# Kernel tuning notes

Hardware: AMD Instinct MI355X
Metric: run time of the kernel (lower is better)

Reference implementation:

```python
import jax, jax.numpy as jnp
import numpy as np

L = 2048      # max_length / encoder sequence length
E = 1024      # eo_hidden_size
H = 1024      # hidden_size
D = 512       # embed_size
V = 32000     # vocab_size
MV = 32768    # max_vocab_size


def setup_inputs() -> dict:
    key = jax.random.key(0)
    ks = jax.random.split(key, 20)
    s = 0.02
    return {
        "inp": jax.random.randint(ks[0], (1,), 0, V),
        "hidden": jax.random.normal(ks[1], (1, 1, H), jnp.float32),
        "encoder_outputs": jax.random.normal(ks[2], (L, E), jnp.float32),
        "input_seq": jax.random.randint(ks[3], (L,), 0, MV),
        "pre_prob": jax.random.randint(ks[4], (L,), 0, 2),
        "emb": jax.random.normal(ks[5], (V, D), jnp.float32) * s,
        "attn_W": jax.random.normal(ks[6], (L, H + D), jnp.float32) * s,
        "attn_b": jnp.zeros((L,), jnp.float32),
        "comb_W": jax.random.normal(ks[7], (H, E + D), jnp.float32) * s,
        "comb_b": jnp.zeros((H,), jnp.float32),
        "W_ih": jax.random.normal(ks[8], (3 * H, H + E), jnp.float32) * s,
        "W_hh": jax.random.normal(ks[9], (3 * H, H), jnp.float32) * s,
        "b_ih": jnp.zeros((3 * H,), jnp.float32),
        "b_hh": jnp.zeros((3 * H,), jnp.float32),
        "Wo_W": jax.random.normal(ks[10], (V, H), jnp.float32) * s,
        "Wo_b": jnp.zeros((V,), jnp.float32),
        "Wc_W": jax.random.normal(ks[11], (H, E), jnp.float32) * s,
        "Wc_b": jnp.zeros((H,), jnp.float32),
    }


def reference(inp, hidden, encoder_outputs, input_seq, pre_prob,
              emb, attn_W, attn_b, comb_W, comb_b,
              W_ih, W_hh, b_ih, b_hh, Wo_W, Wo_b, Wc_W, Wc_b):
    tok = inp[0]
    # --- copy-mechanism selective read (int path, matches torch .long() trunc) ---
    sel_w = (input_seq == tok).astype(jnp.int32) * pre_prob.astype(jnp.int32)  # [L]
    eo_int = jax.lax.stop_gradient(encoder_outputs).astype(jnp.int32)          # trunc toward 0
    sel_reading = (sel_w @ eo_int).astype(jnp.float32)                          # [E]
    # --- embedding (OOV -> UNK id 2); dropout is identity in eval ---
    embed_idx = jnp.where(tok >= V, 2, tok)
    embedded = emb[embed_idx]                                                   # [D]
    h = hidden[0, 0]                                                            # [H]
    # --- attention over encoder outputs ---
    attn_weights = jax.nn.softmax(attn_W @ jnp.concatenate([embedded, h]) + attn_b)  # [L]
    attn_applied = attn_weights @ encoder_outputs                               # [E]
    out = jax.nn.relu(comb_W @ jnp.concatenate([embedded, attn_applied]) + comb_b)   # [H]
    # --- single GRU step (torch gate order: r, z, n) ---
    x = jnp.concatenate([out, sel_reading])                                     # [H+E]
    gi = W_ih @ x + b_ih
    gh = W_hh @ h + b_hh
    r = jax.nn.sigmoid(gi[:H] + gh[:H])
    z = jax.nn.sigmoid(gi[H:2 * H] + gh[H:2 * H])
    n = jnp.tanh(gi[2 * H:] + r * gh[2 * H:])
    h_new = (1.0 - z) * n + z * h                                               # [H]
    # --- generate vs copy scores ---
    score_g = Wo_W @ h_new + Wo_b                                               # [V]
    score_c = jnp.tanh(encoder_outputs @ Wc_W.T + Wc_b) @ h_new                 # [L]
    score = jax.nn.softmax(jnp.concatenate([score_g, score_c]))                 # [V+L]
    prob_g, prob_c = score[:V], score[V:]
    # pad generate probs to MV and scatter-add copy probs (== mm with one-hot)
    out1 = jnp.zeros((MV,), score.dtype).at[:V].set(prob_g)
    out1 = out1.at[input_seq].add(prob_c)
    out1 = jnp.where(out1 == 0, 1e-9, out1)
    out1 = out1.at[2].set(1e-9)
    out1 = jnp.log(out1)
    return (out1[None, :], h_new[None, None, :], attn_weights[None, :], prob_c[None, :])
```

## Files before the change

### kernel.cpp

```cpp
#include <hip/hip_runtime.h>
#include <math.h>

#define LQ 2048
#define EQ 1024
#define HQ 1024
#define DQ 512
#define VQ 32000
#define MVQ 32768

#define OUT1_OFF 0
#define HNEW_OFF 32768
#define AW_OFF   33792
#define PC_OFF   35840

#define PSZ 2097152

typedef __attribute__((ext_vector_type(8))) short short8_t;
typedef __attribute__((ext_vector_type(8))) unsigned short ushort8_t;
typedef __attribute__((ext_vector_type(4))) float floatx4;

__device__ inline float wred(float v) {
    v += __shfl_down(v, 32);
    v += __shfl_down(v, 16);
    v += __shfl_down(v, 8);
    v += __shfl_down(v, 4);
    v += __shfl_down(v, 2);
    v += __shfl_down(v, 1);
    return v;
}
__device__ inline float wred_max(float v) {
    v = fmaxf(v, __shfl_down(v, 32));
    v = fmaxf(v, __shfl_down(v, 16));
    v = fmaxf(v, __shfl_down(v, 8));
    v = fmaxf(v, __shfl_down(v, 4));
    v = fmaxf(v, __shfl_down(v, 2));
    v = fmaxf(v, __shfl_down(v, 1));
    return v;
}
__device__ inline float sigmoidf_(float x) { return 1.0f / (1.0f + expf(-x)); }
__device__ inline unsigned short f2bf(float x) {
    unsigned int u = __float_as_uint(x);
    unsigned int r = (u + 0x7fffu + ((u >> 16) & 1u)) >> 16;
    return (unsigned short)r;
}
__device__ inline float bf2f(unsigned short b) {
    return __uint_as_float(((unsigned int)b) << 16);
}
__device__ __forceinline__ void gload16(const unsigned short* g,
                                        unsigned short* l) {
    __builtin_amdgcn_global_load_lds(
        (const __attribute__((address_space(1))) unsigned int*)g,
        (__attribute__((address_space(3))) unsigned int*)l, 16, 0, 0);
}

__global__ __launch_bounds__(256) void k_split_prep(
    const float* __restrict__ enc, const float* __restrict__ Wc,
    const int* __restrict__ inp, const int* __restrict__ input_seq,
    const int* __restrict__ pre_prob,
    unsigned short* __restrict__ Ah, unsigned short* __restrict__ Al,
    unsigned short* __restrict__ Bh, unsigned short* __restrict__ Bl,
    float* __restrict__ x2)
{
    __shared__ int s_cnt;
    __shared__ int s_list[LQ];
    int tid = threadIdx.x;
    if (blockIdx.x == 1536) {
        if (tid == 0) s_cnt = 0;
        __syncthreads();
        int tok = inp[0];
        for (int l = tid; l < LQ; l += 256) {
            if (input_seq[l] == tok && pre_prob[l] != 0) {
                int p = atomicAdd(&s_cnt, 1);
                s_list[p] = l;
            }
        }
        __syncthreads();
        int nm = s_cnt;
        for (int e = tid; e < EQ; e += 256) {
            int acc = 0;
            for (int j = 0; j < nm; ++j)
                acc += (int)enc[(size_t)s_list[j] * EQ + e];
            x2[HQ + e] = (float)acc;
        }
        return;
    }
    size_t e0 = ((size_t)blockIdx.x * 256 + tid) * 8;
    const float* src;
    unsigned short *hdst, *ldst;
    size_t off;
    if (e0 < (size_t)LQ * EQ) { src = enc; hdst = Ah; ldst = Al; off = e0; }
    else { src = Wc; hdst = Bh; ldst = Bl; off = e0 - (size_t)LQ * EQ; }
    float4 v0 = *(const float4*)(src + off);
    float4 v1 = *(const float4*)(src + off + 4);
    float vv[8] = {v0.x, v0.y, v0.z, v0.w, v1.x, v1.y, v1.z, v1.w};
    ushort8_t H, L;
    #pragma unroll
    for (int k = 0; k < 8; ++k) {
        float x = vv[k];
        unsigned short hb = f2bf(x);
        H[k] = hb;
        L[k] = f2bf(x - bf2f(hb));
    }
    *(ushort8_t*)(hdst + off) = H;
    *(ushort8_t*)(ldst + off) = L;
}

__global__ __launch_bounds__(256, 2) void k_gemm_mfma(
    const unsigned short* __restrict__ Ah, const unsigned short* __restrict__ Al,
    const unsigned short* __restrict__ Bh, const unsigned short* __restrict__ Bl,
    float* __restrict__ P)
{
    __shared__ unsigned short sm[4 * 8192];
    const int t = threadIdx.x;
    const int lane = t & 63, wid = t >> 6;
    const int n0 = blockIdx.x * 128;
    const int m0 = blockIdx.y * 128;
    const int kz = blockIdx.z * 512;
    float* Pz = P + (size_t)blockIdx.z * PSZ;

    const unsigned short* tsrc =
        (wid == 0) ? Ah + (size_t)m0 * EQ :
        (wid == 1) ? Al + (size_t)m0 * EQ :
        (wid == 2) ? Bh + (size_t)n0 * EQ :
                     Bl + (size_t)n0 * EQ;
    unsigned short* tdst = sm + wid * 8192;

    const int srow = lane >> 3;
    const int schunk = lane & 7;
    const int wm = (wid >> 1) * 64, wn = (wid & 1) * 64;
    const int fr = lane & 15, kg = lane >> 4;

    floatx4 acc[4][4];
    #pragma unroll
    for (int i = 0; i < 4; ++i)
        #pragma unroll
        for (int j = 0; j < 4; ++j)
            acc[i][j] = (floatx4){0.f, 0.f, 0.f, 0.f};

    for (int s = 0; s < 8; ++s) {
        #pragma unroll
        for (int c = 0; c < 16; ++c) {
            int row = c * 8 + srow;
            int gch = schunk ^ (row & 7);
            gload16(tsrc + (size_t)row * EQ + kz + s * 64 + gch * 8,
                    tdst + c * 512);
        }
        __syncthreads();
        #pragma unroll
        for (int kk = 0; kk < 2; ++kk) {
            short8_t fah[4], fal[4], fbh[4], fbl[4];
            #pragma unroll
            for (int f = 0; f < 4; ++f) {
                int rowa = wm + f * 16 + fr;
                int ba = rowa * 128 + ((kk * 4 + kg) ^ (rowa & 7)) * 16;
                fah[f] = *(const short8_t*)((const char*)sm + ba);
                fal[f] = *(const short8_t*)((const char*)sm + 16384 + ba);
                int rowb = wn + f * 16 + fr;
                int bb = rowb * 128 + ((kk * 4 + kg) ^ (rowb & 7)) * 16;
                fbh[f] = *(const short8_t*)((const char*)sm + 32768 + bb);
                fbl[f] = *(const short8_t*)((const char*)sm + 49152 + bb);
            }
            #pragma unroll
            for (int i = 0; i < 4; ++i)
                #pragma unroll
                for (int j = 0; j < 4; ++j) {
                    acc[i][j] = __builtin_amdgcn_mfma_f32_16x16x32_bf16(
                        fah[i], fbh[j], acc[i][j], 0, 0, 0);
                    acc[i][j] = __builtin_amdgcn_mfma_f32_16x16x32_bf16(
                        fal[i], fbh[j], acc[i][j], 0, 0, 0);
                    acc[i][j] = __builtin_amdgcn_mfma_f32_16x16x32_bf16(
                        fah[i], fbl[j], acc[i][j], 0, 0, 0);
                }
        }
        __syncthreads();
    }
    #pragma unroll
    for (int i = 0; i < 4; ++i)
        #pragma unroll
        for (int j = 0; j < 4; ++j) {
            int row = m0 + wm + i * 16 + kg * 4;
            int col = n0 + wn + j * 16 + fr;
            #pragma unroll
            for (int r = 0; r < 4; ++r)
                Pz[(size_t)(row + r) * HQ + col] = acc[i][j][r];
        }
}

__global__ __launch_bounds__(256) void k_attn(
    const float* __restrict__ W, const float* __restrict__ b,
    const int* __restrict__ inp, const float* __restrict__ emb,
    const float* __restrict__ hidden, float* __restrict__ logits,
    float* __restrict__ aa)
{
    int t = threadIdx.x;
    if (blockIdx.x < 4) aa[blockIdx.x * 256 + t] = 0.0f;
    int warp = t >> 6, lane = t & 63;
    int r = blockIdx.x * 4 + warp;
    int tok = inp[0];
    int ei = (tok >= VQ) ? 2 : tok;
    const float4* Wr = (const float4*)(W + (size_t)r * 1536);
    const float4* e4 = (const float4*)(emb + (size_t)ei * DQ);
    const float4* h4 = (const float4*)hidden;
    float acc = 0.0f;
    #pragma unroll
    for (int i = 0; i < 6; ++i) {
        int idx = lane + i * 64;
        float4 x = (idx < 128) ? e4[idx] : h4[idx - 128];
        float4 w = Wr[idx];
        acc += w.x * x.x + w.y * x.y + w.z * x.z + w.w * x.w;
    }
    acc = wred(acc);
    if (lane == 0) logits[r] = acc + b[r];
}

__global__ __launch_bounds__(256) void k_attn_sm_apply(
    const float* __restrict__ logits, const float* __restrict__ enc,
    float* __restrict__ aa, float* __restrict__ aw_out)
{
    __shared__ float sred[4];
    __shared__ float s_w[128];
    int tid = threadIdx.x, wid = tid >> 6, lane = tid & 63;
    float m = -3.4e38f;
    for (int i = tid; i < LQ; i += 256) m = fmaxf(m, logits[i]);
    m = wred_max(m);
    if (lane == 0) sred[wid] = m;
    __syncthreads();
    if (tid == 0)
        sred[0] = fmaxf(fmaxf(sred[0], sred[1]), fmaxf(sred[2], sred[3]));
    __syncthreads();
    m = sred[0];
    __syncthreads();
    float s = 0.0f;
    for (int i = tid; i < LQ; i += 256) s += expf(logits[i] - m);
    s = wred(s);
    if (lane == 0) sred[wid] = s;
    __syncthreads();
    if (tid == 0) sred[0] = sred[0] + sred[1] + sred[2] + sred[3];
    __syncthreads();
    s = sred[0];
    int l0 = blockIdx.y * 128;
    if (tid < 128) {
        float w = expf(logits[l0 + tid] - m) / s;
        s_w[tid] = w;
        if (blockIdx.x == 0) aw_out[l0 + tid] = w;
    }
    __syncthreads();
    int e = blockIdx.x * 256 + tid;
    float acc = 0.0f;
    for (int l = 0; l < 128; ++l)
        acc = fmaf(s_w[l], enc[(size_t)(l0 + l) * EQ + e], acc);
    atomicAdd(&aa[e], acc);
}

__global__ __launch_bounds__(256) void k_comb(
    const float* __restrict__ W, const float* __restrict__ b,
    const int* __restrict__ inp, const float* __restrict__ emb,
    const float* __restrict__ aa, float* __restrict__ x2)
{
    int warp = threadIdx.x >> 6, lane = threadIdx.x & 63;
    int r = blockIdx.x * 4 + warp;
    int tok = inp[0];
    int ei = (tok >= VQ) ? 2 : tok;
    const float4* Wr = (const float4*)(W + (size_t)r * 1536);
    const float4* e4 = (const float4*)(emb + (size_t)ei * DQ);
    const float4* a4 = (const float4*)aa;
    float acc = 0.0f;
    #pragma unroll
    for (int i = 0; i < 6; ++i) {
        int idx = lane + i * 64;
        float4 x = (idx < 128) ? e4[idx] : a4[idx - 128];
        float4 w = Wr[idx];
        acc += w.x * x.x + w.y * x.y + w.z * x.z + w.w * x.w;
    }
    acc = wred(acc);
    if (lane == 0) x2[r] = fmaxf(acc + b[r], 0.0f);
}

__global__ __launch_bounds__(256) void k_gru(
    const float* __restrict__ W_ih, const float* __restrict__ W_hh,
    const float* __restrict__ b_ih, const float* __restrict__ b_hh,
    const float* __restrict__ x2, const float* __restrict__ h,
    float* __restrict__ hnew, float* __restrict__ out_h)
{
    int warp = threadIdx.x >> 6, lane = threadIdx.x & 63;
    int i = blockIdx.x * 4 + warp;
    const float4* xv = (const float4*)x2;
    const float4* hv = (const float4*)h;
    const float4* Wr = (const float4*)(W_ih + (size_t)i * 2048);
    const float4* Wz = (const float4*)(W_ih + (size_t)(HQ + i) * 2048);
    const float4* Wn = (const float4*)(W_ih + (size_t)(2 * HQ + i) * 2048);
    const float4* Ur = (const float4*)(W_hh + (size_t)i * 1024);
    const float4* Uz = (const float4*)(W_hh + (size_t)(HQ + i) * 1024);
    const float4* Un = (const float4*)(W_hh + (size_t)(2 * HQ + i) * 1024);
    float ar = 0, az = 0, an = 0, br = 0, bz = 0, bn = 0;
    #pragma unroll
    for (int c = 0; c < 8; ++c) {
        int idx = lane + c * 64;
        float4 x = xv[idx];
        float4 w = Wr[idx]; ar += w.x*x.x + w.y*x.y + w.z*x.z + w.w*x.w;
        w = Wz[idx];        az += w.x*x.x + w.y*x.y + w.z*x.z + w.w*x.w;
        w = Wn[idx];        an += w.x*x.x + w.y*x.y + w.z*x.z + w.w*x.w;
    }
    #pragma unroll
    for (int c = 0; c < 4; ++c) {
        int idx = lane + c * 64;
        float4 x = hv[idx];
        float4 w = Ur[idx]; br += w.x*x.x + w.y*x.y + w.z*x.z + w.w*x.w;
        w = Uz[idx];        bz += w.x*x.x + w.y*x.y + w.z*x.z + w.w*x.w;
        w = Un[idx];        bn += w.x*x.x + w.y*x.y + w.z*x.z + w.w*x.w;
    }
    ar = wred(ar); az = wred(az); an = wred(an);
    br = wred(br); bz = wred(bz); bn = wred(bn);
    if (lane == 0) {
        float r = sigmoidf_(ar + b_ih[i] + br + b_hh[i]);
        float z = sigmoidf_(az + b_ih[HQ + i] + bz + b_hh[HQ + i]);
        float n = tanhf(an + b_ih[2 * HQ + i] + r * (bn + b_hh[2 * HQ + i]));
        float hn = (1.0f - z) * n + z * h[i];
        hnew[i] = hn;
        out_h[i] = hn;
    }
}

__global__ __launch_bounds__(256) void k_scores(
    const float* __restrict__ Wo_W, const float* __restrict__ Wo_b,
    const float* __restrict__ P, const float* __restrict__ Wc_b,
    const float* __restrict__ hnew, float* __restrict__ score)
{
    int warp = threadIdx.x >> 6, lane = threadIdx.x & 63;
    int r = blockIdx.x * 4 + warp;
    const float4* hv = (const float4*)hnew;
    float acc = 0.0f;
    if (r < VQ) {
        const float4* Wr = (const float4*)(Wo_W + (size_t)r * HQ);
        #pragma unroll
        for (int i = 0; i < 4; ++i) {
            int idx = lane + i * 64;
            float4 w = Wr[idx], x = hv[idx];
            acc += w.x * x.x + w.y * x.y + w.z * x.z + w.w * x.w;
        }
        acc = wred(acc);
        if (lane == 0) score[r] = acc + Wo_b[r];
    } else {
        int l = r - VQ;
        const float4* P0 = (const float4*)(P + (size_t)l * HQ);
        const float4* P1 = (const float4*)(P + (size_t)PSZ + (size_t)l * HQ);
        #pragma unroll
        for (int i = 0; i < 4; ++i) {
            int idx = lane + i * 64;
            float4 a = P0[idx], b = P1[idx];
            float4 bb = *(const float4*)(Wc_b + idx * 4);
            float4 x = hv[idx];
            acc += tanhf(a.x + b.x + bb.x) * x.x + tanhf(a.y + b.y + bb.y) * x.y +
                   tanhf(a.z + b.z + bb.z) * x.z + tanhf(a.w + b.w + bb.w) * x.w;
        }
        acc = wred(acc);
        if (lane == 0) score[VQ + l] = acc;
    }
}

__global__ __launch_bounds__(256) void k_probs(
    const float* __restrict__ score, float* __restrict__ out1,
    float* __restrict__ out_pc)
{
    __shared__ float sred[4];
    const int N = VQ + LQ;
    int tid = threadIdx.x, wid = tid >> 6, lane = tid & 63;
    float m = -3.4e38f;
    for (int i = tid; i < N; i += 256) m = fmaxf(m, score[i]);
    m = wred_max(m);
    if (lane == 0) sred[wid] = m;
    __syncthreads();
    if (tid == 0)
        sred[0] = fmaxf(fmaxf(sred[0], sred[1]), fmaxf(sred[2], sred[3]));
    __syncthreads();
    m = sred[0];
    __syncthreads();
    float s = 0.0f;
    for (int i = tid; i < N; i += 256) s += expf(score[i] - m);
    s = wred(s);
    if (lane == 0) sred[wid] = s;
    __syncthreads();
    if (tid == 0) sred[0] = sred[0] + sred[1] + sred[2] + sred[3];
    __syncthreads();
    s = sred[0];
    int i = blockIdx.x * 256 + tid;
    if (i < MVQ) {
        out1[i] = (i < VQ) ? expf(score[i] - m) / s : 0.0f;
    } else {
        int l = i - MVQ;
        out_pc[l] = expf(score[VQ + l] - m) / s;
    }
}

__global__ __launch_bounds__(256) void k_scatter(
    const int* __restrict__ input_seq, const float* __restrict__ pc,
    float* __restrict__ out1)
{
    int l = blockIdx.x * 256 + threadIdx.x;
    atomicAdd(&out1[input_seq[l]], pc[l]);
}

__global__ __launch_bounds__(256) void k_log(float* __restrict__ out1)
{
    int i = blockIdx.x * 256 + threadIdx.x;
    float v = out1[i];
    if (i == 2 || v == 0.0f) v = 1e-9f;
    out1[i] = logf(v);
}

extern "C" void kernel_launch(void* const* d_in, const int* in_sizes, int n_in,
                              void* d_out, int out_size, void* d_ws, size_t ws_size,
                              hipStream_t stream) {
    const int*   inp       = (const int*)  d_in[0];
    const float* hidden    = (const float*)d_in[1];
    const float* enc       = (const float*)d_in[2];
    const int*   input_seq = (const int*)  d_in[3];
    const int*   pre_prob  = (const int*)  d_in[4];
    const float* emb       = (const float*)d_in[5];
    const float* attn_W    = (const float*)d_in[6];
    const float* attn_b    = (const float*)d_in[7];
    const float* comb_W    = (const float*)d_in[8];
    const float* comb_b    = (const float*)d_in[9];
    const float* W_ih      = (const float*)d_in[10];
    const float* W_hh      = (const float*)d_in[11];
    const float* b_ih      = (const float*)d_in[12];
    const float* b_hh      = (const float*)d_in[13];
    const float* Wo_W      = (const float*)d_in[14];
    const float* Wo_b      = (const float*)d_in[15];
    const float* Wc_W      = (const float*)d_in[16];
    const float* Wc_b      = (const float*)d_in[17];

    float* out = (float*)d_out;

    unsigned short* Ah = (unsigned short*)d_ws;
    unsigned short* Al = Ah + (size_t)LQ * EQ;
    unsigned short* Bh = Al + (size_t)LQ * EQ;
    unsigned short* Bl = Bh + (size_t)HQ * EQ;
    float* P      = (float*)(Bl + (size_t)HQ * EQ);
    float* x2     = P + 2 * (size_t)PSZ;
    float* hnew   = x2 + 2048;
    float* logits = hnew + 1024;
    float* aa     = logits + 2048;
    float* score  = aa + 1024;

    k_split_prep<<<1537, 256, 0, stream>>>(enc, Wc_W, inp, input_seq, pre_prob,
                                           Ah, Al, Bh, Bl, x2);
    k_gemm_mfma<<<dim3(HQ / 128, LQ / 128, 2), 256, 0, stream>>>(Ah, Al, Bh, Bl,
                                                                 P);
    k_attn<<<LQ / 4, 256, 0, stream>>>(attn_W, attn_b, inp, emb, hidden,
                                       logits, aa);
    k_attn_sm_apply<<<dim3(EQ / 256, 16), 256, 0, stream>>>(logits, enc, aa,
                                                            out + AW_OFF);
    k_comb<<<HQ / 4, 256, 0, stream>>>(comb_W, comb_b, inp, emb, aa, x2);
    k_gru<<<HQ / 4, 256, 0, stream>>>(W_ih, W_hh, b_ih, b_hh, x2, hidden,
                                      hnew, out + HNEW_OFF);
    k_scores<<<(VQ + LQ) / 4, 256, 0, stream>>>(Wo_W, Wo_b, P, Wc_b, hnew,
                                                score);
    k_probs<<<(MVQ + LQ) / 256, 256, 0, stream>>>(score, out + OUT1_OFF,
                                                  out + PC_OFF);
    k_scatter<<<LQ / 256, 256, 0, stream>>>(input_seq, out + PC_OFF,
                                            out + OUT1_OFF);
    k_log<<<MVQ / 256, 256, 0, stream>>>(out + OUT1_OFF);
}
```

Before: 131.8 us.

## Fuse attention logits into prep, split GEMM K four ways, merge softmax/scatter/log

Folds the attention-logit GEMV into the prep kernel as extra blocks, which removes one launch. The encoder GEMM K-split rises from 2 to 4 slices so the grid has more blocks, and the score kernel sums four partial buffers. The probability, scatter and log kernels are merged into one kernel. Each block builds its own shared-memory histogram of copy probabilities by scanning the full input_seq, so every block now repeats that scan. The split also costs more partial-buffer memory traffic.

```diff
diff --git a/kernel.cpp b/kernel.cpp
--- a/kernel.cpp
+++ b/kernel.cpp
@@ -14,6 +14,7 @@
 #define PC_OFF   35840
 
 #define PSZ 2097152
+#define KSPLIT 4
 
 typedef __attribute__((ext_vector_type(8))) short short8_t;
 typedef __attribute__((ext_vector_type(8))) unsigned short ushort8_t;
@@ -53,18 +54,42 @@
         (__attribute__((address_space(3))) unsigned int*)l, 16, 0, 0);
 }
 
-__global__ __launch_bounds__(256) void k_split_prep(
+__global__ __launch_bounds__(256) void k_prep(
     const float* __restrict__ enc, const float* __restrict__ Wc,
     const int* __restrict__ inp, const int* __restrict__ input_seq,
     const int* __restrict__ pre_prob,
+    const float* __restrict__ attn_W, const float* __restrict__ attn_b,
+    const float* __restrict__ emb, const float* __restrict__ hidden,
     unsigned short* __restrict__ Ah, unsigned short* __restrict__ Al,
     unsigned short* __restrict__ Bh, unsigned short* __restrict__ Bl,
-    float* __restrict__ x2)
+    float* __restrict__ x2, float* __restrict__ logits, float* __restrict__ aa)
 {
     __shared__ int s_cnt;
     __shared__ int s_list[LQ];
-    int tid = threadIdx.x;
-    if (blockIdx.x == 1536) {
+    const int tid = threadIdx.x;
+    const int bx = blockIdx.x;
+    if (bx < 512) {
+        if (bx < 4) aa[bx * 256 + tid] = 0.0f;
+        int warp = tid >> 6, lane = tid & 63;
+        int r = bx * 4 + warp;
+        int tok = inp[0];
+        int ei = (tok >= VQ) ? 2 : tok;
+        const float4* Wr = (const float4*)(attn_W + (size_t)r * 1536);
+        const float4* e4 = (const float4*)(emb + (size_t)ei * DQ);
+        const float4* h4 = (const float4*)hidden;
+        float acc = 0.0f;
+        #pragma unroll
+        for (int i = 0; i < 6; ++i) {
+            int idx = lane + i * 64;
+            float4 x = (idx < 128) ? e4[idx] : h4[idx - 128];
+            float4 w = Wr[idx];
+            acc += w.x * x.x + w.y * x.y + w.z * x.z + w.w * x.w;
+        }
+        acc = wred(acc);
+        if (lane == 0) logits[r] = acc + attn_b[r];
+        return;
+    }
+    if (bx == 512) {
         if (tid == 0) s_cnt = 0;
         __syncthreads();
         int tok = inp[0];
@@ -84,7 +109,7 @@
         }
         return;
     }
-    size_t e0 = ((size_t)blockIdx.x * 256 + tid) * 8;
+    size_t e0 = ((size_t)(bx - 513) * 256 + tid) * 8;
     const float* src;
     unsigned short *hdst, *ldst;
     size_t off;
@@ -115,7 +140,7 @@
     const int lane = t & 63, wid = t >> 6;
     const int n0 = blockIdx.x * 128;
     const int m0 = blockIdx.y * 128;
-    const int kz = blockIdx.z * 512;
+    const int kz = blockIdx.z * 256;
     float* Pz = P + (size_t)blockIdx.z * PSZ;
 
     const unsigned short* tsrc =
@@ -137,7 +162,7 @@
         for (int j = 0; j < 4; ++j)
             acc[i][j] = (floatx4){0.f, 0.f, 0.f, 0.f};
 
-    for (int s = 0; s < 8; ++s) {
+    for (int s = 0; s < 4; ++s) {
         #pragma unroll
         for (int c = 0; c < 16; ++c) {
             int row = c * 8 + srow;
@@ -186,33 +211,6 @@
         }
 }
 
-__global__ __launch_bounds__(256) void k_attn(
-    const float* __restrict__ W, const float* __restrict__ b,
-    const int* __restrict__ inp, const float* __restrict__ emb,
-    const float* __restrict__ hidden, float* __restrict__ logits,
-    float* __restrict__ aa)
-{
-    int t = threadIdx.x;
-    if (blockIdx.x < 4) aa[blockIdx.x * 256 + t] = 0.0f;
-    int warp = t >> 6, lane = t & 63;
-    int r = blockIdx.x * 4 + warp;
-    int tok = inp[0];
-    int ei = (tok >= VQ) ? 2 : tok;
-    const float4* Wr = (const float4*)(W + (size_t)r * 1536);
-    const float4* e4 = (const float4*)(emb + (size_t)ei * DQ);
-    const float4* h4 = (const float4*)hidden;
-    float acc = 0.0f;
-    #pragma unroll
-    for (int i = 0; i < 6; ++i) {
-        int idx = lane + i * 64;
-        float4 x = (idx < 128) ? e4[idx] : h4[idx - 128];
-        float4 w = Wr[idx];
-        acc += w.x * x.x + w.y * x.y + w.z * x.z + w.w * x.w;
-    }
-    acc = wred(acc);
-    if (lane == 0) logits[r] = acc + b[r];
-}
-
 __global__ __launch_bounds__(256) void k_attn_sm_apply(
     const float* __restrict__ logits, const float* __restrict__ enc,
     float* __restrict__ aa, float* __restrict__ aw_out)
@@ -344,25 +342,30 @@
         int l = r - VQ;
         const float4* P0 = (const float4*)(P + (size_t)l * HQ);
         const float4* P1 = (const float4*)(P + (size_t)PSZ + (size_t)l * HQ);
+        const float4* P2 = (const float4*)(P + 2 * (size_t)PSZ + (size_t)l * HQ);
+        const float4* P3 = (const float4*)(P + 3 * (size_t)PSZ + (size_t)l * HQ);
         #pragma unroll
         for (int i = 0; i < 4; ++i) {
             int idx = lane + i * 64;
-            float4 a = P0[idx], b = P1[idx];
+            float4 a = P0[idx], b1 = P1[idx], b2 = P2[idx], b3 = P3[idx];
             float4 bb = *(const float4*)(Wc_b + idx * 4);
             float4 x = hv[idx];
-            acc += tanhf(a.x + b.x + bb.x) * x.x + tanhf(a.y + b.y + bb.y) * x.y +
-                   tanhf(a.z + b.z + bb.z) * x.z + tanhf(a.w + b.w + bb.w) * x.w;
+            acc += tanhf(a.x + b1.x + b2.x + b3.x + bb.x) * x.x +
+                   tanhf(a.y + b1.y + b2.y + b3.y + bb.y) * x.y +
+                   tanhf(a.z + b1.z + b2.z + b3.z + bb.z) * x.z +
+                   tanhf(a.w + b1.w + b2.w + b3.w + bb.w) * x.w;
         }
         acc = wred(acc);
         if (lane == 0) score[VQ + l] = acc;
     }
 }
 
-__global__ __launch_bounds__(256) void k_probs(
-    const float* __restrict__ score, float* __restrict__ out1,
-    float* __restrict__ out_pc)
+__global__ __launch_bounds__(256) void k_final(
+    const float* __restrict__ score, const int* __restrict__ input_seq,
+    float* __restrict__ out1, float* __restrict__ out_pc)
 {
     __shared__ float sred[4];
+    __shared__ float bins[256];
     const int N = VQ + LQ;
     int tid = threadIdx.x, wid = tid >> 6, lane = tid & 63;
     float m = -3.4e38f;
@@ -383,27 +386,21 @@
     if (tid == 0) sred[0] = sred[0] + sred[1] + sred[2] + sred[3];
     __syncthreads();
     s = sred[0];
-    int i = blockIdx.x * 256 + tid;
-    if (i < MVQ) {
-        out1[i] = (i < VQ) ? expf(score[i] - m) / s : 0.0f;
-    } else {
-        int l = i - MVQ;
+    bins[tid] = 0.0f;
+    __syncthreads();
+    int i0 = blockIdx.x * 256;
+    for (int l = tid; l < LQ; l += 256) {
+        int si = input_seq[l];
+        if (si >= i0 && si < i0 + 256)
+            atomicAdd(&bins[si - i0], expf(score[VQ + l] - m) / s);
+    }
+    if (blockIdx.x < 8) {
+        int l = blockIdx.x * 256 + tid;
         out_pc[l] = expf(score[VQ + l] - m) / s;
     }
-}
-
-__global__ __launch_bounds__(256) void k_scatter(
-    const int* __restrict__ input_seq, const float* __restrict__ pc,
-    float* __restrict__ out1)
-{
-    int l = blockIdx.x * 256 + threadIdx.x;
-    atomicAdd(&out1[input_seq[l]], pc[l]);
-}
-
-__global__ __launch_bounds__(256) void k_log(float* __restrict__ out1)
-{
-    int i = blockIdx.x * 256 + threadIdx.x;
-    float v = out1[i];
+    __syncthreads();
+    int i = i0 + tid;
+    float v = ((i < VQ) ? expf(score[i] - m) / s : 0.0f) + bins[tid];
     if (i == 2 || v == 0.0f) v = 1e-9f;
     out1[i] = logf(v);
 }
@@ -437,18 +434,17 @@
     unsigned short* Bh = Al + (size_t)LQ * EQ;
     unsigned short* Bl = Bh + (size_t)HQ * EQ;
     float* P      = (float*)(Bl + (size_t)HQ * EQ);
-    float* x2     = P + 2 * (size_t)PSZ;
+    float* x2     = P + (size_t)KSPLIT * PSZ;
     float* hnew   = x2 + 2048;
     float* logits = hnew + 1024;
     float* aa     = logits + 2048;
     float* score  = aa + 1024;
 
-    k_split_prep<<<1537, 256, 0, stream>>>(enc, Wc_W, inp, input_seq, pre_prob,
-                                           Ah, Al, Bh, Bl, x2);
-    k_gemm_mfma<<<dim3(HQ / 128, LQ / 128, 2), 256, 0, stream>>>(Ah, Al, Bh, Bl,
-                                                                 P);
-    k_attn<<<LQ / 4, 256, 0, stream>>>(attn_W, attn_b, inp, emb, hidden,
-                                       logits, aa);
+    k_prep<<<2049, 256, 0, stream>>>(enc, Wc_W, inp, input_seq, pre_prob,
+                                     attn_W, attn_b, emb, hidden,
+                                     Ah, Al, Bh, Bl, x2, logits, aa);
+    k_gemm_mfma<<<dim3(HQ / 128, LQ / 128, KSPLIT), 256, 0, stream>>>(
+        Ah, Al, Bh, Bl, P);
     k_attn_sm_apply<<<dim3(EQ / 256, 16), 256, 0, stream>>>(logits, enc, aa,
                                                             out + AW_OFF);
     k_comb<<<HQ / 4, 256, 0, stream>>>(comb_W, comb_b, inp, emb, aa, x2);
@@ -456,9 +452,6 @@
                                       hnew, out + HNEW_OFF);
     k_scores<<<(VQ + LQ) / 4, 256, 0, stream>>>(Wo_W, Wo_b, P, Wc_b, hnew,
                                                 score);
-    k_probs<<<(MVQ + LQ) / 256, 256, 0, stream>>>(score, out + OUT1_OFF,
-                                                  out + PC_OFF);
-    k_scatter<<<LQ / 256, 256, 0, stream>>>(input_seq, out + PC_OFF,
-                                            out + OUT1_OFF);
-    k_log<<<MVQ / 256, 256, 0, stream>>>(out + OUT1_OFF);
-}
+    k_final<<<MVQ / 256, 256, 0, stream>>>(score, input_seq, out + OUT1_OFF,
+                                           out + PC_OFF);
+}
```

Measured after the change: 124.0 us. 1.06x faster.
